# Kernel tuning notes

Measured on AMD Instinct MI355X. Metric: run time of the kernel, lower is better.

The kernel has to match this reference:

```python
import jax, jax.numpy as jnp
import numpy as np

V = 50000   # words_num
D = 128     # embedding_dim
B = 2048    # batch
P = 20      # max Huffman path length


def setup_inputs() -> dict:
    key = jax.random.key(0)
    k1, k2, k3, k4, k5 = jax.random.split(key, 5)
    inputs_vector = jax.random.uniform(k1, (B, V), dtype=jnp.float32)
    path_nodes_indices = jax.random.randint(k2, (B, P), 0, V)
    huffman_codes = jax.random.randint(k3, (B, P), 0, 2).astype(jnp.float32)
    mask = jnp.ones((B, P), dtype=jnp.float32)
    # learned params, torch nn.Linear weight layout [out, in], kaiming-uniform-ish scale
    W_emb = jax.random.uniform(k4, (D, V), dtype=jnp.float32, minval=-1.0, maxval=1.0) / np.sqrt(V)
    W_cls = jax.random.uniform(k5, (V, D), dtype=jnp.float32, minval=-1.0, maxval=1.0) / np.sqrt(D)
    return {
        "inputs_vector": inputs_vector,
        "W_emb": W_emb,
        "W_cls": W_cls,
        "path_nodes_indices": path_nodes_indices,
        "huffman_codes": huffman_codes,
        "mask": mask,
    }


def _bce_with_logits(logits, targets):
    # numerically stable, elementwise (reduction='none')
    return jnp.maximum(logits, 0.0) - logits * targets + jnp.log1p(jnp.exp(-jnp.abs(logits)))


def reference(inputs_vector, W_emb, W_cls, path_nodes_indices, huffman_codes, mask):
    x = inputs_vector @ W_emb.T              # [B, D]  embedding Linear (no bias)
    logits_full = x @ W_cls.T                # [B, V]  full-vocab cls matmul (as in source)
    logits = jnp.take_along_axis(logits_full, path_nodes_indices, axis=1)  # [B, P]
    loss = _bce_with_logits(logits, huffman_codes)  # [B, P]
    masked_loss = loss * mask
    per_sample = masked_loss.sum(axis=-1) / mask.sum(axis=-1)  # [B]
    return per_sample.mean()
```

## Files before the change

### kernel.cpp

```cpp
#include <hip/hip_runtime.h>
#include <hip/hip_bf16.h>

#define V 50000
#define D 128
#define B 2048
#define P 20

#define BM 128
#define BN 128
#define BK 64
#define NSPLIT 56
#define KC 896
#define NMT (B / BM)

typedef float  f32x4   __attribute__((ext_vector_type(4)));
typedef short  bf16x8  __attribute__((ext_vector_type(8)));
typedef unsigned int uint4v __attribute__((ext_vector_type(4)));

__device__ __forceinline__ unsigned int pk2(float a, float b) {
    return (__float_as_uint(b) & 0xFFFF0000u) | (__float_as_uint(a) >> 16);
}
__device__ __forceinline__ unsigned short f2bf(float f) {
    unsigned int u = __float_as_uint(f);
    return (unsigned short)((u + 0x7FFFu + ((u >> 16) & 1u)) >> 16);
}

__global__ __launch_bounds__(256, 4)
void w2v_gemm_splitk(const float* __restrict__ Ain, const float* __restrict__ Wemb,
                     void* __restrict__ part, int use_atomic) {
    __shared__ unsigned short Sm[2 * BM * BK];
    unsigned short* As = Sm;
    unsigned short* Ws = Sm + BM * BK;

    const int i     = blockIdx.x;
    const int xcd   = i & 7;
    const int j     = i >> 3;
    const int s     = xcd * 7 + (j >> 4);
    const int mtile = j & 15;
    const int m0    = mtile * BM;
    const int k0    = s * KC;
    const int k1    = (k0 + KC < V) ? (k0 + KC) : V;

    const int tid  = threadIdx.x;
    const int lane = tid & 63;
    const int wid  = tid >> 6;
    const int wr   = wid >> 1;
    const int wc   = wid & 1;

    f32x4 acc[4][4] = {};

    for (int ks = k0; ks < k1; ks += BK) {
#pragma unroll
        for (int t = 0; t < 8; ++t) {
            const int slot = tid + (t & 3) * 256;
            const int row  = slot >> 3;
            const int c8   = slot & 7;
            const int kg   = ks + c8 * 8;
            f32x4 v0 = {0.f, 0.f, 0.f, 0.f};
            f32x4 v1 = {0.f, 0.f, 0.f, 0.f};
            if (kg < k1) {
                if (t < 4) {
                    const f32x4* src = reinterpret_cast<const f32x4*>(&Ain[(size_t)(m0 + row) * V + kg]);
                    v0 = __builtin_nontemporal_load(src);
                    v1 = __builtin_nontemporal_load(src + 1);
                } else {
                    const f32x4* src = reinterpret_cast<const f32x4*>(&Wemb[(size_t)row * V + kg]);
                    v0 = src[0];
                    v1 = src[1];
                }
            }
            uint4v u;
            u.x = pk2(v0[0], v0[1]);
            u.y = pk2(v0[2], v0[3]);
            u.z = pk2(v1[0], v1[1]);
            u.w = pk2(v1[2], v1[3]);
            const unsigned dst = (unsigned)(row * 128) + (((unsigned)(c8 * 16)) ^ ((unsigned)(row & 7) << 4));
            char* base = (t < 4) ? (char*)As : (char*)Ws;
            *reinterpret_cast<uint4v*>(base + dst) = u;
        }
        __syncthreads();

#pragma unroll
        for (int kk = 0; kk < BK; kk += 32) {
            const unsigned kb = (unsigned)(kk * 2) + ((unsigned)(lane >> 4) << 4);
            bf16x8 af[4], wf[4];
#pragma unroll
            for (int m = 0; m < 4; ++m) {
                const int r = wr * 64 + m * 16 + (lane & 15);
                af[m] = *reinterpret_cast<const bf16x8*>((char*)As + r * 128 + (kb ^ ((unsigned)(r & 7) << 4)));
            }
#pragma unroll
            for (int n = 0; n < 4; ++n) {
                const int r = wc * 64 + n * 16 + (lane & 15);
                wf[n] = *reinterpret_cast<const bf16x8*>((char*)Ws + r * 128 + (kb ^ ((unsigned)(r & 7) << 4)));
            }
#pragma unroll
            for (int m = 0; m < 4; ++m)
#pragma unroll
                for (int n = 0; n < 4; ++n)
                    acc[m][n] = __builtin_amdgcn_mfma_f32_16x16x32_bf16(af[m], wf[n], acc[m][n], 0, 0, 0);
        }
        __syncthreads();
    }

    if (use_atomic) {
        float* outp = (float*)part;
#pragma unroll
        for (int m = 0; m < 4; ++m) {
            int r0 = m0 + wr * 64 + m * 16 + (lane >> 4) * 4;
#pragma unroll
            for (int n = 0; n < 4; ++n) {
                int c0 = wc * 64 + n * 16 + (lane & 15);
#pragma unroll
                for (int jj = 0; jj < 4; ++jj)
                    atomicAdd(&outp[(size_t)(r0 + jj) * D + c0], acc[m][n][jj]);
            }
        }
        return;
    }
#pragma unroll
    for (int m = 0; m < 4; ++m) {
        int r0 = wr * 64 + m * 16 + (lane >> 4) * 4;
#pragma unroll
        for (int n = 0; n < 4; ++n) {
            int c0 = wc * 64 + n * 16 + (lane & 15);
#pragma unroll
            for (int jj = 0; jj < 4; ++jj)
                Sm[(r0 + jj) * 128 + c0] = f2bf(acc[m][n][jj]);
        }
    }
    __syncthreads();
    char* dstb = (char*)part + ((size_t)s * B + m0) * (D * 2);
#pragma unroll
    for (int it = 0; it < 8; ++it) {
        const int off = (it * 256 + tid) * 16;
        uint4v v = *reinterpret_cast<const uint4v*>((char*)Sm + off);
        __builtin_nontemporal_store(v, reinterpret_cast<uint4v*>(dstb + off));
    }
}

__global__ __launch_bounds__(256)
void w2v_loss(const void* __restrict__ part, int nsplit, int part_bf16,
              const float* __restrict__ Wcls, const int* __restrict__ pathIdx,
              const float* __restrict__ codes, const float* __restrict__ mask,
              float* __restrict__ out) {
    const int lane = threadIdx.x & 63;
    const int wid  = threadIdx.x >> 6;
    const int b    = blockIdx.x * 4 + wid;

    float x0 = 0.f, x1 = 0.f;
    if (part_bf16) {
        const unsigned* pb = (const unsigned*)part;
        for (int s = 0; s < nsplit; ++s) {
            unsigned u = __builtin_nontemporal_load(&pb[((size_t)s * B + b) * 64 + lane]);
            x0 += __uint_as_float(u << 16);
            x1 += __uint_as_float(u & 0xFFFF0000u);
        }
    } else {
        const float* pf = (const float*)part;
        const float2 v = *reinterpret_cast<const float2*>(&pf[(size_t)b * D + lane * 2]);
        x0 = v.x; x1 = v.y;
    }

    float lsum = 0.f, msum = 0.f;
#pragma unroll
    for (int p = 0; p < P; ++p) {
        int node = pathIdx[b * P + p];
        const float2 w = *reinterpret_cast<const float2*>(&Wcls[(size_t)node * D + lane * 2]);
        float d = x0 * w.x + x1 * w.y;
#pragma unroll
        for (int off = 1; off < 64; off <<= 1)
            d += __shfl_xor(d, off, 64);
        float t  = codes[b * P + p];
        float mm = mask[b * P + p];
        float loss = fmaxf(d, 0.f) - d * t + log1pf(__expf(-fabsf(d)));
        lsum += loss * mm;
        msum += mm;
    }
    float per = (msum > 0.f) ? (lsum / msum) : 0.f;

    __shared__ float wsum[4];
    if (lane == 0) wsum[wid] = per;
    __syncthreads();
    if (threadIdx.x == 0) {
        float ssum = wsum[0] + wsum[1] + wsum[2] + wsum[3];
        atomicAdd(out, ssum * (1.0f / (float)B));
    }
}

extern "C" void kernel_launch(void* const* d_in, const int* in_sizes, int n_in,
                              void* d_out, int out_size, void* d_ws, size_t ws_size,
                              hipStream_t stream) {
    const float* inputs = (const float*)d_in[0];
    const float* W_emb  = (const float*)d_in[1];
    const float* W_cls  = (const float*)d_in[2];
    const int*   path   = (const int*)  d_in[3];
    const float* codes  = (const float*)d_in[4];
    const float* mask   = (const float*)d_in[5];
    float* out = (float*)d_out;

    const size_t part_need = (size_t)NSPLIT * B * D * sizeof(unsigned short);
    const int use_atomic = (ws_size < part_need) ? 1 : 0;
    const int nsplit_eff = use_atomic ? 1 : NSPLIT;

    if (use_atomic)
        hipMemsetAsync(d_ws, 0, (size_t)B * D * sizeof(float), stream);
    hipMemsetAsync(d_out, 0, sizeof(float), stream);

    w2v_gemm_splitk<<<dim3(NMT * NSPLIT), dim3(256), 0, stream>>>(inputs, W_emb, d_ws, use_atomic);
    w2v_loss<<<dim3(B / 4), dim3(256), 0, stream>>>(d_ws, nsplit_eff, use_atomic ? 0 : 1,
                                                    W_cls, path, codes, mask, out);
}
```

Measured before the change: 175.2 us.

## Load activations directly into registers and pre-cast W_emb to bf16

The GEMM kernel is restructured to 512-thread blocks with BM=256. Each wave loads its activation rows straight from global memory into MFMA fragments, skipping LDS staging, and only W_emb goes through shared memory. A separate pre-pass converts W_emb to bf16 once per call, which halves W traffic across the 8 M-tiles but adds a kernel launch and an extra read and write of W. The split-K count changes to 64, and nontemporal hints are dropped on the partial stores and loads, so the loss kernel now sums 64 partials.

```diff
diff --git a/kernel.cpp b/kernel.cpp
--- a/kernel.cpp
+++ b/kernel.cpp
@@ -6,11 +6,10 @@
 #define B 2048
 #define P 20
 
-#define BM 128
-#define BN 128
+#define BM 256
 #define BK 64
-#define NSPLIT 56
-#define KC 896
+#define NSPLIT 64
+#define KC 784
 #define NMT (B / BM)
 
 typedef float  f32x4   __attribute__((ext_vector_type(4)));
@@ -24,81 +23,121 @@
     unsigned int u = __float_as_uint(f);
     return (unsigned short)((u + 0x7FFFu + ((u >> 16) & 1u)) >> 16);
 }
-
-__global__ __launch_bounds__(256, 4)
-void w2v_gemm_splitk(const float* __restrict__ Ain, const float* __restrict__ Wemb,
-                     void* __restrict__ part, int use_atomic) {
-    __shared__ unsigned short Sm[2 * BM * BK];
-    unsigned short* As = Sm;
-    unsigned short* Ws = Sm + BM * BK;
-
-    const int i     = blockIdx.x;
-    const int xcd   = i & 7;
-    const int j     = i >> 3;
-    const int s     = xcd * 7 + (j >> 4);
-    const int mtile = j & 15;
-    const int m0    = mtile * BM;
-    const int k0    = s * KC;
-    const int k1    = (k0 + KC < V) ? (k0 + KC) : V;
+__device__ __forceinline__ bf16x8 pack8(f32x4 lo, f32x4 hi) {
+    union { uint4v u; bf16x8 h; } r;
+    r.u.x = pk2(lo[0], lo[1]); r.u.y = pk2(lo[2], lo[3]);
+    r.u.z = pk2(hi[0], hi[1]); r.u.w = pk2(hi[2], hi[3]);
+    return r.h;
+}
+
+__global__ __launch_bounds__(256)
+void w2v_wcast(const float* __restrict__ Wemb, unsigned* __restrict__ Wb) {
+    const size_t t = (size_t)blockIdx.x * 256 + threadIdx.x;
+    const size_t base = t * 8;
+    if (base >= (size_t)D * V) return;
+    const f32x4* src = reinterpret_cast<const f32x4*>(Wemb + base);
+    f32x4 v0 = src[0], v1 = src[1];
+    uint4v u;
+    u.x = pk2(v0[0], v0[1]); u.y = pk2(v0[2], v0[3]);
+    u.z = pk2(v1[0], v1[1]); u.w = pk2(v1[2], v1[3]);
+    *reinterpret_cast<uint4v*>(Wb + base / 2) = u;
+}
+
+template<int WBF>
+__global__ __launch_bounds__(512, 4)
+void w2v_gemm(const float* __restrict__ Ain, const void* __restrict__ Wsrc,
+              void* __restrict__ part, int use_atomic) {
+    __shared__ uint4v smem4[4096];
+    char* smem = (char*)smem4;
+
+    const int i   = blockIdx.x;
+    const int xcd = i & 7;
+    const int j   = i >> 3;
+    const int s   = xcd * 8 + (j >> 3);
+    const int mt  = j & 7;
+    const int m0  = mt * BM;
+    const int k0  = s * KC;
+    const int k1  = (k0 + KC < V) ? (k0 + KC) : V;
 
     const int tid  = threadIdx.x;
     const int lane = tid & 63;
     const int wid  = tid >> 6;
-    const int wr   = wid >> 1;
-    const int wc   = wid & 1;
-
-    f32x4 acc[4][4] = {};
+    const int fr   = lane & 15;
+    const int kg4  = lane >> 4;
+
+    f32x4 acc[2][8] = {};
+
+    const float* Arow0 = Ain + (size_t)(m0 + wid * 32 + fr) * V;
+    const float* Arow1 = Arow0 + (size_t)16 * V;
 
     for (int ks = k0; ks < k1; ks += BK) {
 #pragma unroll
-        for (int t = 0; t < 8; ++t) {
-            const int slot = tid + (t & 3) * 256;
-            const int row  = slot >> 3;
+        for (int t2 = 0; t2 < 2; ++t2) {
+            const int slot = tid + t2 * 512;
+            const int d    = slot >> 3;
             const int c8   = slot & 7;
             const int kg   = ks + c8 * 8;
-            f32x4 v0 = {0.f, 0.f, 0.f, 0.f};
-            f32x4 v1 = {0.f, 0.f, 0.f, 0.f};
+            uint4v u = {0u, 0u, 0u, 0u};
             if (kg < k1) {
-                if (t < 4) {
-                    const f32x4* src = reinterpret_cast<const f32x4*>(&Ain[(size_t)(m0 + row) * V + kg]);
-                    v0 = __builtin_nontemporal_load(src);
-                    v1 = __builtin_nontemporal_load(src + 1);
+                if (WBF) {
+                    u = *reinterpret_cast<const uint4v*>(
+                        (const unsigned short*)Wsrc + (size_t)d * V + kg);
                 } else {
-                    const f32x4* src = reinterpret_cast<const f32x4*>(&Wemb[(size_t)row * V + kg]);
-                    v0 = src[0];
-                    v1 = src[1];
+                    const f32x4* sp = reinterpret_cast<const f32x4*>(
+                        (const float*)Wsrc + (size_t)d * V + kg);
+                    f32x4 v0 = sp[0], v1 = sp[1];
+                    u.x = pk2(v0[0], v0[1]); u.y = pk2(v0[2], v0[3]);
+                    u.z = pk2(v1[0], v1[1]); u.w = pk2(v1[2], v1[3]);
                 }
             }
-            uint4v u;
-            u.x = pk2(v0[0], v0[1]);
-            u.y = pk2(v0[2], v0[3]);
-            u.z = pk2(v1[0], v1[1]);
-            u.w = pk2(v1[2], v1[3]);
-            const unsigned dst = (unsigned)(row * 128) + (((unsigned)(c8 * 16)) ^ ((unsigned)(row & 7) << 4));
-            char* base = (t < 4) ? (char*)As : (char*)Ws;
-            *reinterpret_cast<uint4v*>(base + dst) = u;
+            const unsigned dst = (unsigned)(d * 128) +
+                (((unsigned)(c8 * 16)) ^ ((unsigned)(d & 7) << 4));
+            *reinterpret_cast<uint4v*>(smem + dst) = u;
+        }
+
+        const int koff = ks + kg4 * 8;
+        f32x4 a00l = {0,0,0,0}, a00h = {0,0,0,0}, a01l = {0,0,0,0}, a01h = {0,0,0,0};
+        f32x4 a10l = {0,0,0,0}, a10h = {0,0,0,0}, a11l = {0,0,0,0}, a11h = {0,0,0,0};
+        {
+            const f32x4* p0 = reinterpret_cast<const f32x4*>(Arow0 + koff);
+            const f32x4* p1 = reinterpret_cast<const f32x4*>(Arow1 + koff);
+            a00l = p0[0]; a00h = p0[1];
+            a01l = p1[0]; a01h = p1[1];
+        }
+        const bool kh1v = (ks + 32 < k1);
+        if (kh1v) {
+            const f32x4* p0 = reinterpret_cast<const f32x4*>(Arow0 + koff + 32);
+            const f32x4* p1 = reinterpret_cast<const f32x4*>(Arow1 + koff + 32);
+            a10l = p0[0]; a10h = p0[1];
+            a11l = p1[0]; a11h = p1[1];
         }
         __syncthreads();
 
-#pragma unroll
-        for (int kk = 0; kk < BK; kk += 32) {
-            const unsigned kb = (unsigned)(kk * 2) + ((unsigned)(lane >> 4) << 4);
-            bf16x8 af[4], wf[4];
-#pragma unroll
-            for (int m = 0; m < 4; ++m) {
-                const int r = wr * 64 + m * 16 + (lane & 15);
-                af[m] = *reinterpret_cast<const bf16x8*>((char*)As + r * 128 + (kb ^ ((unsigned)(r & 7) << 4)));
-            }
-#pragma unroll
-            for (int n = 0; n < 4; ++n) {
-                const int r = wc * 64 + n * 16 + (lane & 15);
-                wf[n] = *reinterpret_cast<const bf16x8*>((char*)Ws + r * 128 + (kb ^ ((unsigned)(r & 7) << 4)));
-            }
-#pragma unroll
-            for (int m = 0; m < 4; ++m)
-#pragma unroll
-                for (int n = 0; n < 4; ++n)
-                    acc[m][n] = __builtin_amdgcn_mfma_f32_16x16x32_bf16(af[m], wf[n], acc[m][n], 0, 0, 0);
+        {
+            const bf16x8 af0 = pack8(a00l, a00h);
+            const bf16x8 af1 = pack8(a01l, a01h);
+            const unsigned kb = (unsigned)kg4 << 4;
+#pragma unroll
+            for (int n = 0; n < 8; ++n) {
+                const int r = n * 16 + fr;
+                const bf16x8 wf = *reinterpret_cast<const bf16x8*>(
+                    smem + r * 128 + (kb ^ ((unsigned)(r & 7) << 4)));
+                acc[0][n] = __builtin_amdgcn_mfma_f32_16x16x32_bf16(af0, wf, acc[0][n], 0, 0, 0);
+                acc[1][n] = __builtin_amdgcn_mfma_f32_16x16x32_bf16(af1, wf, acc[1][n], 0, 0, 0);
+            }
+        }
+        if (kh1v) {
+            const bf16x8 af0 = pack8(a10l, a10h);
+            const bf16x8 af1 = pack8(a11l, a11h);
+            const unsigned kb = 64u + ((unsigned)kg4 << 4);
+#pragma unroll
+            for (int n = 0; n < 8; ++n) {
+                const int r = n * 16 + fr;
+                const bf16x8 wf = *reinterpret_cast<const bf16x8*>(
+                    smem + r * 128 + (kb ^ ((unsigned)(r & 7) << 4)));
+                acc[0][n] = __builtin_amdgcn_mfma_f32_16x16x32_bf16(af0, wf, acc[0][n], 0, 0, 0);
+                acc[1][n] = __builtin_amdgcn_mfma_f32_16x16x32_bf16(af1, wf, acc[1][n], 0, 0, 0);
+            }
         }
         __syncthreads();
     }
@@ -106,11 +145,11 @@
     if (use_atomic) {
         float* outp = (float*)part;
 #pragma unroll
-        for (int m = 0; m < 4; ++m) {
-            int r0 = m0 + wr * 64 + m * 16 + (lane >> 4) * 4;
-#pragma unroll
-            for (int n = 0; n < 4; ++n) {
-                int c0 = wc * 64 + n * 16 + (lane & 15);
+        for (int m = 0; m < 2; ++m) {
+            const int r0 = m0 + wid * 32 + m * 16 + kg4 * 4;
+#pragma unroll
+            for (int n = 0; n < 8; ++n) {
+                const int c0 = n * 16 + fr;
 #pragma unroll
                 for (int jj = 0; jj < 4; ++jj)
                     atomicAdd(&outp[(size_t)(r0 + jj) * D + c0], acc[m][n][jj]);
@@ -118,24 +157,25 @@
         }
         return;
     }
-#pragma unroll
-    for (int m = 0; m < 4; ++m) {
-        int r0 = wr * 64 + m * 16 + (lane >> 4) * 4;
-#pragma unroll
-        for (int n = 0; n < 4; ++n) {
-            int c0 = wc * 64 + n * 16 + (lane & 15);
+    unsigned short* Cs = (unsigned short*)smem;
+#pragma unroll
+    for (int m = 0; m < 2; ++m) {
+        const int r0 = wid * 32 + m * 16 + kg4 * 4;
+#pragma unroll
+        for (int n = 0; n < 8; ++n) {
+            const int c0 = n * 16 + fr;
 #pragma unroll
             for (int jj = 0; jj < 4; ++jj)
-                Sm[(r0 + jj) * 128 + c0] = f2bf(acc[m][n][jj]);
+                Cs[(r0 + jj) * 128 + c0] = f2bf(acc[m][n][jj]);
         }
     }
     __syncthreads();
     char* dstb = (char*)part + ((size_t)s * B + m0) * (D * 2);
 #pragma unroll
     for (int it = 0; it < 8; ++it) {
-        const int off = (it * 256 + tid) * 16;
-        uint4v v = *reinterpret_cast<const uint4v*>((char*)Sm + off);
-        __builtin_nontemporal_store(v, reinterpret_cast<uint4v*>(dstb + off));
+        const int off = (it * 512 + tid) * 16;
+        uint4v v = *reinterpret_cast<const uint4v*>(smem + off);
+        *reinterpret_cast<uint4v*>(dstb + off) = v;
     }
 }
 
@@ -152,7 +192,7 @@
     if (part_bf16) {
         const unsigned* pb = (const unsigned*)part;
         for (int s = 0; s < nsplit; ++s) {
-            unsigned u = __builtin_nontemporal_load(&pb[((size_t)s * B + b) * 64 + lane]);
+            unsigned u = pb[((size_t)s * B + b) * 64 + lane];
             x0 += __uint_as_float(u << 16);
             x1 += __uint_as_float(u & 0xFFFF0000u);
         }
@@ -199,15 +239,23 @@
     const float* mask   = (const float*)d_in[5];
     float* out = (float*)d_out;
 
-    const size_t part_need = (size_t)NSPLIT * B * D * sizeof(unsigned short);
-    const int use_atomic = (ws_size < part_need) ? 1 : 0;
-    const int nsplit_eff = use_atomic ? 1 : NSPLIT;
-
-    if (use_atomic)
+    hipMemsetAsync(d_out, 0, sizeof(float), stream);
+
+    const size_t wb_bytes  = (size_t)D * V * 2;
+    const size_t part_off  = (wb_bytes + 255) & ~(size_t)255;
+    const size_t part_need = part_off + (size_t)NSPLIT * B * D * 2;
+
+    if (ws_size >= part_need) {
+        unsigned* Wb  = (unsigned*)d_ws;
+        char* partp   = (char*)d_ws + part_off;
+        w2v_wcast<<<dim3((D * V / 8 + 255) / 256), dim3(256), 0, stream>>>(W_emb, Wb);
+        w2v_gemm<1><<<dim3(NMT * NSPLIT), dim3(512), 0, stream>>>(inputs, Wb, partp, 0);
+        w2v_loss<<<dim3(B / 4), dim3(256), 0, stream>>>(partp, NSPLIT, 1,
+                                                        W_cls, path, codes, mask, out);
+    } else {
         hipMemsetAsync(d_ws, 0, (size_t)B * D * sizeof(float), stream);
-    hipMemsetAsync(d_out, 0, sizeof(float), stream);
-
-    w2v_gemm_splitk<<<dim3(NMT * NSPLIT), dim3(256), 0, stream>>>(inputs, W_emb, d_ws, use_atomic);
-    w2v_loss<<<dim3(B / 4), dim3(256), 0, stream>>>(d_ws, nsplit_eff, use_atomic ? 0 : 1,
-                                                    W_cls, path, codes, mask, out);
-}
+        w2v_gemm<0><<<dim3(NMT * NSPLIT), dim3(512), 0, stream>>>(inputs, W_emb, d_ws, 1);
+        w2v_loss<<<dim3(B / 4), dim3(256), 0, stream>>>(d_ws, 1, 0,
+                                                        W_cls, path, codes, mask, out);
+    }
+}
```

After: 153.0 us. -12.6%, faster.
